# Kernel tuning notes

Hardware: AMD Instinct MI355X
Metric: run time of the kernel (lower is better)

## Reference

```python
import jax, jax.numpy as jnp
import numpy as np
from math import sqrt

D_MODEL = 1024
HEADS = 16
D_K = D_MODEL // HEADS
NEG = -1e9


def setup_inputs() -> dict:
    key = jax.random.key(0)
    ks = jax.random.split(key, 8)
    bs, s, d = 2, 2048, D_MODEL
    inp = {
        "k": jax.random.normal(ks[0], (bs, s, d), jnp.float32),
        "v": jax.random.normal(ks[1], (bs, s, d), jnp.float32),
        "q": jax.random.normal(ks[2], (bs, s, d), jnp.float32),
        "mask": jax.random.randint(ks[3], (bs, s, 1), 0, 2).astype(jnp.int64),
        # torch nn.Linear weights: y = x @ W.T, W is [out, in]
        "Wq": jax.random.normal(ks[4], (d, d), jnp.float32) / sqrt(d),
        "Wk": jax.random.normal(ks[5], (d, d), jnp.float32) / sqrt(d),
        "Wv": jax.random.normal(ks[6], (d, d), jnp.float32) / sqrt(d),
        "Wo": jax.random.normal(ks[7], (d, d), jnp.float32) / sqrt(d),
    }
    return inp


def reference(k, v, q, mask, Wq, Wk, Wv, Wo):
    bs, s_k, d = k.shape
    s_q = q.shape[1]
    h, d_k = HEADS, D_K
    # linear projections (no bias), then split heads -> [bs, h, s, d_k]
    kh = (k @ Wk.T).reshape(bs, s_k, h, d_k).transpose(0, 2, 1, 3)
    vh = (v @ Wv.T).reshape(bs, s_k, h, d_k).transpose(0, 2, 1, 3)
    qh = (q @ Wq.T).reshape(bs, s_q, h, d_k).transpose(0, 2, 1, 3)
    # scaled dot-product scores [bs, h, s_q, s_k]
    scores = jnp.einsum("bhqd,bhkd->bhqk", qh, kh) / sqrt(d_k)
    # mask [bs, s_k, 1] -> [bs, 1, 1, s_k], masked positions get -1e9
    m = mask[:, None].transpose(0, 1, 3, 2)  # [bs,1,1,s_k]
    scores = jnp.where(m == 0, NEG, scores)
    probs = jax.nn.softmax(scores, axis=-1)  # dropout is identity (eval)
    attn = jnp.einsum("bhqk,bhkd->bhqd", probs, vh)
    attn_concat = attn.transpose(0, 2, 1, 3).reshape(bs, s_q, d)
    return attn_concat @ Wo.T
```

## Files before the change

kernel.cpp:

```cpp
#include <hip/hip_runtime.h>

typedef __bf16 bf16x8 __attribute__((ext_vector_type(8)));
typedef float f32x4 __attribute__((ext_vector_type(4)));

#define BS 2
#define SEQ 2048
#define DM 1024
#define NH 16
#define DKH 64
#define GM 4096
#define GN 1024
#define GK 1024
#define NEGV (-1e9f)

#define OFF_XQ 0u
#define OFF_XK 4194304u
#define OFF_XV 8388608u
#define OFF_WQ 12582912u
#define OFF_WK 13631488u
#define OFF_WV 14680064u
#define OFF_WO 15728640u
#define OFF_QH 16777216u
#define OFF_KC 20971520u
#define OFF_VT 25165824u
#define OFF_AT OFF_XQ

#if __has_builtin(__builtin_amdgcn_exp2f)
#define EXP2(x) __builtin_amdgcn_exp2f(x)
#else
static __device__ __forceinline__ float EXP2(float x) {
    float r;
    asm volatile("v_exp_f32 %0, %1" : "=v"(r) : "v"(x));
    return r;
}
#endif

__device__ __forceinline__ unsigned cvt_pk(float lo, float hi) {
    unsigned r;
    asm volatile("v_cvt_pk_bf16_f32 %0, %1, %2" : "=v"(r) : "v"(lo), "v"(hi));
    return r;
}

__device__ __forceinline__ unsigned short f2b(float f) {
    unsigned u = __builtin_bit_cast(unsigned, f);
    u += 0x7fffu + ((u >> 16) & 1u);
    return (unsigned short)(u >> 16);
}

typedef const __attribute__((address_space(1))) unsigned int* gas_t;
typedef __attribute__((address_space(3))) unsigned int* las_t;

__device__ __forceinline__ void gload_lds16(const ushort* g, ushort* l) {
    __builtin_amdgcn_global_load_lds((gas_t)(const void*)g, (las_t)(void*)l, 16, 0, 0);
}

#define BARRIER() __builtin_amdgcn_s_barrier()
#define VMCNT(n) asm volatile("s_waitcnt vmcnt(" #n ")" ::: "memory")

__global__ __launch_bounds__(256)
void cvt_kernel(const float* __restrict__ q, const float* __restrict__ k,
                const float* __restrict__ v, const float* __restrict__ wq,
                const float* __restrict__ wk, const float* __restrict__ wv,
                const float* __restrict__ wo, ushort* __restrict__ ws)
{
    const float* src; unsigned n; unsigned dst;
    switch (blockIdx.y) {
        case 0: src = q;  n = 4194304u; dst = OFF_XQ; break;
        case 1: src = k;  n = 4194304u; dst = OFF_XK; break;
        case 2: src = v;  n = 4194304u; dst = OFF_XV; break;
        case 3: src = wq; n = 1048576u; dst = OFF_WQ; break;
        case 4: src = wk; n = 1048576u; dst = OFF_WK; break;
        case 5: src = wv; n = 1048576u; dst = OFF_WV; break;
        default: src = wo; n = 1048576u; dst = OFF_WO; break;
    }
    unsigned i = (blockIdx.x * 256u + threadIdx.x) * 4u;
    if (i >= n) return;
    float4 f = *(const float4*)(src + i);
    ushort4 o;
    o.x = f2b(f.x); o.y = f2b(f.y); o.z = f2b(f.z); o.w = f2b(f.w);
    *(ushort4*)(ws + dst + i) = o;
}

__global__ __launch_bounds__(256)
void scan_kernel(const int* __restrict__ mask, int* __restrict__ cpos, int* __restrict__ mbuf)
{
    const int b = blockIdx.x;
    const int* mp = mask + (size_t)b * SEQ;
    const int tid = threadIdx.x;
    const int lane = tid & 63, w = tid >> 6;
    int v[8];
    int cnt = 0;
#pragma unroll
    for (int j = 0; j < 8; ++j) { v[j] = mp[tid * 8 + j]; cnt += (v[j] != 0); }
    int inc = cnt;
#pragma unroll
    for (int d = 1; d < 64; d <<= 1) {
        int t = __shfl_up(inc, d);
        if (lane >= d) inc += t;
    }
    __shared__ int wsum[4];
    if (lane == 63) wsum[w] = inc;
    __syncthreads();
    int base = inc - cnt;
    for (int i = 0; i < w; ++i) base += wsum[i];
    int c = base;
    int* ob = cpos + (size_t)b * SEQ;
#pragma unroll
    for (int j = 0; j < 8; ++j) {
        ob[tid * 8 + j] = (v[j] != 0) ? c : -1;
        c += (v[j] != 0);
    }
    if (tid == 255) mbuf[b] = base + cnt;
}

__global__ __launch_bounds__(512)
void gemm256(const ushort* __restrict__ Abase, const ushort* __restrict__ Bbase,
             ushort* __restrict__ wsbase, const int* __restrict__ cpos)
{
    __shared__ __align__(16) ushort lA[2][2][8192];
    __shared__ __align__(16) ushort lB[2][2][8192];

    const unsigned z = blockIdx.z;
    const ushort* A  = Abase + (size_t)z * (GM * GK);
    const ushort* Bw = Bbase + (size_t)z * (GN * GK);
    const float scale = (z == 0) ? 0.125f * 1.44269504088896f : 1.0f;

    const int tid = threadIdx.x;
    const int lane = tid & 63, wid = tid >> 6;
    const int wr = wid >> 2, wc = wid & 3;
    const int lr = lane & 15, lg = lane >> 4;
    const int srow8 = lane >> 3, scol = lane & 7;

    const int lin = blockIdx.y * 4 + blockIdx.x;
    const int xcd = lin & 7, kidx = lin >> 3;
    const int m0 = (xcd * 2 + (kidx >> 2)) * 256;
    const int n0 = (kidx & 3) * 256;

    f32x4 acc[8][4] = {};
    bf16x8 aq[4][2], aq2[4][2], b01[2][2], b23[2][2];

#define STAGE_A(s, h, t)                                                          \
    _Pragma("unroll") for (int c = 0; c < 2; ++c) {                               \
        int rih = (wid * 2 + c) * 8 + srow8;                                      \
        gload_lds16(A + (size_t)(m0 + (h) * 128 + rih) * GK + (t) * 64 +          \
                        ((scol ^ (rih & 7)) * 8),                                 \
                    &lA[s][h][(wid * 2 + c) * 512]);                              \
    }
#define STAGE_B(s, h, t)                                                          \
    _Pragma("unroll") for (int c = 0; c < 2; ++c) {                               \
        int rih = (wid * 2 + c) * 8 + srow8;                                      \
        gload_lds16(Bw + (size_t)(n0 + (h) * 128 + rih) * GK + (t) * 64 +         \
                         ((scol ^ (rih & 7)) * 8),                                \
                    &lB[s][h][(wid * 2 + c) * 512]);                              \
    }
#define LDA_FRAG(dst, s, ibase)                                                   \
    _Pragma("unroll") for (int i2 = 0; i2 < 4; ++i2)                              \
    _Pragma("unroll") for (int kk = 0; kk < 2; ++kk) {                            \
        int row = ((ibase) + i2) * 16 + lr;                                       \
        dst[i2][kk] = *(const bf16x8*)&lA[s][wr][row * 64 +                       \
                          (((kk * 4 + lg) ^ (row & 7)) * 8)];                     \
    }
#define LDB_FRAG(dst, s, jbase)                                                   \
    _Pragma("unroll") for (int j2 = 0; j2 < 2; ++j2)                              \
    _Pragma("unroll") for (int kk = 0; kk < 2; ++kk) {                            \
        int row = (wc & 1) * 64 + ((jbase) + j2) * 16 + lr;                       \
        dst[j2][kk] = *(const bf16x8*)&lB[s][wc >> 1][row * 64 +                  \
                          (((kk * 4 + lg) ^ (row & 7)) * 8)];                     \
    }
#define MMA_Q(ibase, jbase, av, bv)                                               \
    __builtin_amdgcn_s_setprio(1);                                                \
    _Pragma("unroll") for (int i2 = 0; i2 < 4; ++i2)                              \
    _Pragma("unroll") for (int j2 = 0; j2 < 2; ++j2)                              \
    _Pragma("unroll") for (int kk = 0; kk < 2; ++kk)                              \
        acc[(ibase) + i2][(jbase) + j2] = __builtin_amdgcn_mfma_f32_16x16x32_bf16(\
            av[i2][kk], bv[j2][kk], acc[(ibase) + i2][(jbase) + j2], 0, 0, 0);    \
    __builtin_amdgcn_s_setprio(0);

    STAGE_B(0, 0, 0); STAGE_B(0, 1, 0); STAGE_A(0, 0, 0); STAGE_A(0, 1, 0);
    STAGE_B(1, 0, 1); STAGE_B(1, 1, 1); STAGE_A(1, 0, 1); STAGE_A(1, 1, 1);
    VMCNT(8);
    BARRIER();

    for (int it = 0; it < 7; ++it) {
        const int t2 = 2 * it + 2, t3 = 2 * it + 3;
        LDA_FRAG(aq, 0, 0); LDB_FRAG(b01, 0, 0);
        BARRIER(); MMA_Q(0, 0, aq, b01); BARRIER();
        LDB_FRAG(b23, 0, 2);
        BARRIER(); MMA_Q(0, 2, aq, b23); BARRIER();
        LDA_FRAG(aq2, 0, 4);
        STAGE_B(0, 0, t2); STAGE_B(0, 1, t2);
        BARRIER(); MMA_Q(4, 2, aq2, b23); BARRIER();
        STAGE_A(0, 0, t2);
        VMCNT(6);
        BARRIER(); MMA_Q(4, 0, aq2, b01); BARRIER();
        LDA_FRAG(aq, 1, 0); LDB_FRAG(b01, 1, 0);
        STAGE_A(0, 1, t2);
        BARRIER(); MMA_Q(0, 0, aq, b01); BARRIER();
        LDB_FRAG(b23, 1, 2);
        BARRIER(); MMA_Q(0, 2, aq, b23); BARRIER();
        LDA_FRAG(aq2, 1, 4);
        STAGE_B(1, 0, t3); STAGE_B(1, 1, t3);
        BARRIER(); MMA_Q(4, 2, aq2, b23); BARRIER();
        STAGE_A(1, 0, t3); STAGE_A(1, 1, t3);
        VMCNT(8);
        BARRIER(); MMA_Q(4, 0, aq2, b01); BARRIER();
    }

    LDA_FRAG(aq, 0, 0); LDB_FRAG(b01, 0, 0);
    BARRIER(); MMA_Q(0, 0, aq, b01); BARRIER();
    LDB_FRAG(b23, 0, 2);
    BARRIER(); MMA_Q(0, 2, aq, b23); BARRIER();
    LDA_FRAG(aq2, 0, 4);
    BARRIER(); MMA_Q(4, 2, aq2, b23); BARRIER();
    VMCNT(0);
    BARRIER(); MMA_Q(4, 0, aq2, b01); BARRIER();
    LDA_FRAG(aq, 1, 0); LDB_FRAG(b01, 1, 0);
    BARRIER(); MMA_Q(0, 0, aq, b01); BARRIER();
    LDB_FRAG(b23, 1, 2);
    BARRIER(); MMA_Q(0, 2, aq, b23); BARRIER();
    LDA_FRAG(aq2, 1, 4);
    BARRIER(); MMA_Q(4, 2, aq2, b23); BARRIER();
    BARRIER(); MMA_Q(4, 0, aq2, b01); BARRIER();

    ushort* qh  = wsbase + OFF_QH;
    ushort* kc  = wsbase + OFF_KC;
    ushort* vtp = wsbase + OFF_VT;
#pragma unroll
    for (int i = 0; i < 8; ++i) {
#pragma unroll
        for (int r = 0; r < 4; ++r) {
            int row = m0 + wr * 128 + i * 16 + lg * 4 + r;
            int b = row >> 11, s = row & 2047;
            if (z == 0) {
#pragma unroll
                for (int j = 0; j < 4; ++j) {
                    int col = n0 + wc * 64 + j * 16 + lr;
                    qh[(((size_t)b * NH + (col >> 6)) * SEQ + s) * DKH + (col & 63)] =
                        f2b(acc[i][j][r] * scale);
                }
            } else {
                int c = cpos[b * SEQ + s];
                if (c >= 0) {
                    if (z == 1) {
#pragma unroll
                        for (int j = 0; j < 4; ++j) {
                            int col = n0 + wc * 64 + j * 16 + lr;
                            kc[(((size_t)b * NH + (col >> 6)) * SEQ + c) * DKH + (col & 63)] =
                                f2b(acc[i][j][r]);
                        }
                    } else {
                        int vt = (c & ~63) | ((c & 15) * 4 + ((c >> 4) & 3));
#pragma unroll
                        for (int j = 0; j < 4; ++j) {
                            int col = n0 + wc * 64 + j * 16 + lr;
                            vtp[(((size_t)b * NH + (col >> 6)) * DKH + (col & 63)) * SEQ + vt] =
                                f2b(acc[i][j][r]);
                        }
                    }
                }
            }
        }
    }
#undef STAGE_A
#undef STAGE_B
#undef LDA_FRAG
#undef LDB_FRAG
#undef MMA_Q
}

__global__ __launch_bounds__(256)
void gemm_bt(const ushort* __restrict__ A, const ushort* __restrict__ Bw,
             float* __restrict__ of)
{
    __shared__ __align__(16) ushort lA[128 * 64];
    __shared__ __align__(16) ushort lB[128 * 64];

    const int tid = threadIdx.x;
    const int lane = tid & 63, wid = tid >> 6;
    const int wr = wid >> 1, wc = wid & 1;
    const int lr = lane & 15, lg = lane >> 4;
    const int lin = blockIdx.y * 8 + blockIdx.x;
    const int swz = (lin & 7) * 32 + (lin >> 3);
    const int m0 = (swz >> 3) * 128, n0 = (swz & 7) * 128;
    const int srow = wid * 32 + (lane >> 3);
    const int scol = (lane & 7) * 8;

    f32x4 acc[4][4] = {};

    for (int k0 = 0; k0 < GK; k0 += 64) {
        __syncthreads();
#pragma unroll
        for (int p = 0; p < 4; ++p) {
            gload_lds16(A + (size_t)(m0 + srow + p * 8) * GK + k0 + scol,
                        &lA[(wid * 32 + p * 8) * 64]);
            gload_lds16(Bw + (size_t)(n0 + srow + p * 8) * GK + k0 + scol,
                        &lB[(wid * 32 + p * 8) * 64]);
        }
        __syncthreads();
#pragma unroll
        for (int kk = 0; kk < 2; ++kk) {
            bf16x8 af[4], bfr[4];
#pragma unroll
            for (int i = 0; i < 4; ++i) {
                af[i]  = *(const bf16x8*)(&lA[(wr * 64 + i * 16 + lr) * 64 + kk * 32 + lg * 8]);
                bfr[i] = *(const bf16x8*)(&lB[(wc * 64 + i * 16 + lr) * 64 + kk * 32 + lg * 8]);
            }
#pragma unroll
            for (int i = 0; i < 4; ++i)
#pragma unroll
                for (int j = 0; j < 4; ++j)
                    acc[i][j] = __builtin_amdgcn_mfma_f32_16x16x32_bf16(af[i], bfr[j], acc[i][j], 0, 0, 0);
        }
    }

#pragma unroll
    for (int i = 0; i < 4; ++i)
#pragma unroll
        for (int j = 0; j < 4; ++j) {
            int col = n0 + wc * 64 + j * 16 + lr;
#pragma unroll
            for (int r = 0; r < 4; ++r) {
                int row = m0 + wr * 64 + i * 16 + lg * 4 + r;
                of[(size_t)row * GN + col] = acc[i][j][r];
            }
        }
}

__global__ __launch_bounds__(256)
void attn_kernel(ushort* __restrict__ ws, const int* __restrict__ mbuf)
{
    const int bid = blockIdx.x;
    const int qt = bid & 15;
    const int h  = (bid >> 4) & 15;
    const int b  = bid >> 8;
    const int bh = b * NH + h;

    const ushort* Qp = ws + OFF_QH + (size_t)bh * (SEQ * DKH);
    const ushort* Kc = ws + OFF_KC + (size_t)bh * (SEQ * DKH);
    const ushort* VT = ws + OFF_VT + (size_t)bh * (DKH * SEQ);
    ushort* At = ws + OFF_AT;

    const int mb = mbuf[b];
    const int nt = (mb + 63) >> 6;

    __shared__ __align__(16) ushort lK[2][64 * 64];
    __shared__ __align__(16) ushort lV[2][64 * 64];
    __shared__ __align__(16) ushort lP[4][32][72];

    const int tid = threadIdx.x;
    const int lane = tid & 63, wid = tid >> 6;
    const int lr = lane & 15, lg = lane >> 4;
    ushort* lPw = &lP[wid][0][0];

    const int srow = wid * 16 + (lane >> 3);
    const int sg = lane & 7;

    const int qrow0 = qt * 128 + wid * 32;
    bf16x8 qf[2][2];
#pragma unroll
    for (int fr = 0; fr < 2; ++fr)
#pragma unroll
        for (int kk = 0; kk < 2; ++kk)
            qf[fr][kk] = *(const bf16x8*)(Qp + (size_t)(qrow0 + fr * 16 + lr) * DKH + kk * 32 + lg * 8);

    f32x4 acc_o[2][4] = {};
    float lrun[2][4] = {};

    auto STAGE = [&](int buf, int kt) {
        const int kbase = kt * 64;
#pragma unroll
        for (int c = 0; c < 2; ++c) {
            int r = srow + c * 8;
            gload_lds16(Kc + (size_t)(kbase + r) * DKH + ((sg ^ (r & 7)) * 8),
                        &lK[buf][(wid * 16 + c * 8) * 64]);
            gload_lds16(VT + (size_t)r * SEQ + kbase + ((sg ^ (r & 7)) * 8),
                        &lV[buf][(wid * 16 + c * 8) * 64]);
        }
    };

    STAGE(0, 0);
    __syncthreads();

    for (int kt = 0; kt < nt; ++kt) {
        const int cur = kt & 1;
        if (kt + 1 < nt) STAGE(cur ^ 1, kt + 1);
        const ushort* lKc = lK[cur];
        const ushort* lVc = lV[cur];

        f32x4 s[2][4];
        __builtin_amdgcn_s_setprio(1);
#pragma unroll
        for (int fc = 0; fc < 4; ++fc) {
            int row = fc * 16 + lr;
            int sw = row & 7;
            bf16x8 kf0 = *(const bf16x8*)(lKc + row * 64 + ((lg ^ sw) * 8));
            bf16x8 kf1 = *(const bf16x8*)(lKc + row * 64 + (((4 + lg) ^ sw) * 8));
#pragma unroll
            for (int fr = 0; fr < 2; ++fr) {
                f32x4 t = {};
                t = __builtin_amdgcn_mfma_f32_16x16x32_bf16(qf[fr][0], kf0, t, 0, 0, 0);
                t = __builtin_amdgcn_mfma_f32_16x16x32_bf16(qf[fr][1], kf1, t, 0, 0, 0);
                s[fr][fc] = t;
            }
        }
        __builtin_amdgcn_s_setprio(0);

        if (kt == nt - 1) {
            const int kbase = kt * 64;
#pragma unroll
            for (int fc = 0; fc < 4; ++fc)
                if (kbase + fc * 16 + lr >= mb)
#pragma unroll
                    for (int fr = 0; fr < 2; ++fr)
                        s[fr][fc] = f32x4{NEGV, NEGV, NEGV, NEGV};
        }

#pragma unroll
        for (int fr = 0; fr < 2; ++fr)
#pragma unroll
            for (int r = 0; r < 4; ++r) {
                float p0 = EXP2(s[fr][0][r]), p1 = EXP2(s[fr][1][r]);
                float p2 = EXP2(s[fr][2][r]), p3 = EXP2(s[fr][3][r]);
                lrun[fr][r] += (p0 + p1) + (p2 + p3);
                uint2 pk;
                pk.x = cvt_pk(p0, p1);
                pk.y = cvt_pk(p2, p3);
                *(uint2*)(lPw + (fr * 16 + lg * 4 + r) * 72 + lr * 4) = pk;
            }

        __builtin_amdgcn_s_setprio(1);
#pragma unroll
        for (int kk = 0; kk < 2; ++kk) {
            bf16x8 pf[2];
#pragma unroll
            for (int fr = 0; fr < 2; ++fr)
                pf[fr] = *(const bf16x8*)(lPw + (fr * 16 + lr) * 72 + kk * 32 + lg * 8);
#pragma unroll
            for (int fc2 = 0; fc2 < 4; ++fc2) {
                int d = fc2 * 16 + lr;
                bf16x8 vf = *(const bf16x8*)(lVc + d * 64 + (((kk * 4 + lg) ^ (d & 7)) * 8));
#pragma unroll
                for (int fr = 0; fr < 2; ++fr)
                    acc_o[fr][fc2] = __builtin_amdgcn_mfma_f32_16x16x32_bf16(pf[fr], vf, acc_o[fr][fc2], 0, 0, 0);
            }
        }
        __builtin_amdgcn_s_setprio(0);
        __syncthreads();
    }

#pragma unroll
    for (int fr = 0; fr < 2; ++fr)
#pragma unroll
        for (int r = 0; r < 4; ++r) {
            float l = lrun[fr][r];
            l += __shfl_xor(l, 1);
            l += __shfl_xor(l, 2);
            l += __shfl_xor(l, 4);
            l += __shfl_xor(l, 8);
            float rl = 1.0f / l;
            int qrow = qrow0 + fr * 16 + lg * 4 + r;
#pragma unroll
            for (int fc2 = 0; fc2 < 4; ++fc2)
                At[((size_t)(b * SEQ) + qrow) * DM + h * DKH + fc2 * 16 + lr] =
                    f2b(acc_o[fr][fc2][r] * rl);
        }
}

extern "C" void kernel_launch(void* const* d_in, const int* in_sizes, int n_in,
                              void* d_out, int out_size, void* d_ws, size_t ws_size,
                              hipStream_t stream) {
    const float* kin = (const float*)d_in[0];
    const float* vin = (const float*)d_in[1];
    const float* qin = (const float*)d_in[2];
    const int*   msk = (const int*)d_in[3];
    const float* wq  = (const float*)d_in[4];
    const float* wk  = (const float*)d_in[5];
    const float* wv  = (const float*)d_in[6];
    const float* wo  = (const float*)d_in[7];
    ushort* ws = (ushort*)d_ws;
    float* out = (float*)d_out;
    int* cposb = (int*)d_out;
    int* mbuf = cposb + BS * SEQ;

    scan_kernel<<<2, 256, 0, stream>>>(msk, cposb, mbuf);
    cvt_kernel<<<dim3(4096, 7), 256, 0, stream>>>(qin, kin, vin, wq, wk, wv, wo, ws);
    gemm256<<<dim3(4, 16, 3), 512, 0, stream>>>(ws + OFF_XQ, ws + OFF_WQ, ws, cposb);
    attn_kernel<<<512, 256, 0, stream>>>(ws, mbuf);
    gemm_bt<<<dim3(8, 32), 256, 0, stream>>>(ws + OFF_AT, ws + OFF_WO, out);
}
```

Measured before the change: 128.6 us.

## Fuse mask scan into convert kernel and load attention K/V directly from global

Merges the mask prefix-scan into the fp32-to-bf16 conversion kernel as an extra grid row, which removes one launch, and widens conversion to 8 elements per thread using packed conversion. The attention kernel drops LDS staging of K and V, the double buffering and the per-tile barriers, and instead reads MFMA fragments straight from global memory, relying on cache reuse. It also swizzles the block index so that co-scheduled blocks share heads, and removes the setprio hints. Reading K/V directly from global trades LDS traffic and synchronisation for possibly higher-latency global loads that are not software pipelined.

After: 168.1 us. 1.31x slower.

```diff
diff --git a/kernel.cpp b/kernel.cpp
--- a/kernel.cpp
+++ b/kernel.cpp
@@ -58,11 +58,44 @@
 #define VMCNT(n) asm volatile("s_waitcnt vmcnt(" #n ")" ::: "memory")
 
 __global__ __launch_bounds__(256)
-void cvt_kernel(const float* __restrict__ q, const float* __restrict__ k,
-                const float* __restrict__ v, const float* __restrict__ wq,
-                const float* __restrict__ wk, const float* __restrict__ wv,
-                const float* __restrict__ wo, ushort* __restrict__ ws)
+void cvt_scan(const float* __restrict__ q, const float* __restrict__ k,
+              const float* __restrict__ v, const float* __restrict__ wq,
+              const float* __restrict__ wk, const float* __restrict__ wv,
+              const float* __restrict__ wo, ushort* __restrict__ ws,
+              const int* __restrict__ mask, int* __restrict__ cpos,
+              int* __restrict__ mbuf)
 {
+    const int tid = threadIdx.x;
+    if (blockIdx.y == 7) {
+        if (blockIdx.x >= 2) return;
+        const int b = blockIdx.x;
+        const int* mp = mask + (size_t)b * SEQ;
+        const int lane = tid & 63, w = tid >> 6;
+        int vv[8];
+        int cnt = 0;
+#pragma unroll
+        for (int j = 0; j < 8; ++j) { vv[j] = mp[tid * 8 + j]; cnt += (vv[j] != 0); }
+        int inc = cnt;
+#pragma unroll
+        for (int d = 1; d < 64; d <<= 1) {
+            int t = __shfl_up(inc, d);
+            if (lane >= d) inc += t;
+        }
+        __shared__ int wsum[4];
+        if (lane == 63) wsum[w] = inc;
+        __syncthreads();
+        int base = inc - cnt;
+        for (int i = 0; i < w; ++i) base += wsum[i];
+        int c = base;
+        int* ob = cpos + (size_t)b * SEQ;
+#pragma unroll
+        for (int j = 0; j < 8; ++j) {
+            ob[tid * 8 + j] = (vv[j] != 0) ? c : -1;
+            c += (vv[j] != 0);
+        }
+        if (tid == 255) mbuf[b] = base + cnt;
+        return;
+    }
     const float* src; unsigned n; unsigned dst;
     switch (blockIdx.y) {
         case 0: src = q;  n = 4194304u; dst = OFF_XQ; break;
@@ -73,44 +106,16 @@
         case 5: src = wv; n = 1048576u; dst = OFF_WV; break;
         default: src = wo; n = 1048576u; dst = OFF_WO; break;
     }
-    unsigned i = (blockIdx.x * 256u + threadIdx.x) * 4u;
+    unsigned i = (blockIdx.x * 256u + tid) * 8u;
     if (i >= n) return;
-    float4 f = *(const float4*)(src + i);
-    ushort4 o;
-    o.x = f2b(f.x); o.y = f2b(f.y); o.z = f2b(f.z); o.w = f2b(f.w);
-    *(ushort4*)(ws + dst + i) = o;
-}
-
-__global__ __launch_bounds__(256)
-void scan_kernel(const int* __restrict__ mask, int* __restrict__ cpos, int* __restrict__ mbuf)
-{
-    const int b = blockIdx.x;
-    const int* mp = mask + (size_t)b * SEQ;
-    const int tid = threadIdx.x;
-    const int lane = tid & 63, w = tid >> 6;
-    int v[8];
-    int cnt = 0;
-#pragma unroll
-    for (int j = 0; j < 8; ++j) { v[j] = mp[tid * 8 + j]; cnt += (v[j] != 0); }
-    int inc = cnt;
-#pragma unroll
-    for (int d = 1; d < 64; d <<= 1) {
-        int t = __shfl_up(inc, d);
-        if (lane >= d) inc += t;
-    }
-    __shared__ int wsum[4];
-    if (lane == 63) wsum[w] = inc;
-    __syncthreads();
-    int base = inc - cnt;
-    for (int i = 0; i < w; ++i) base += wsum[i];
-    int c = base;
-    int* ob = cpos + (size_t)b * SEQ;
-#pragma unroll
-    for (int j = 0; j < 8; ++j) {
-        ob[tid * 8 + j] = (v[j] != 0) ? c : -1;
-        c += (v[j] != 0);
-    }
-    if (tid == 255) mbuf[b] = base + cnt;
+    float4 f0 = *(const float4*)(src + i);
+    float4 f1 = *(const float4*)(src + i + 4);
+    uint4 o;
+    o.x = cvt_pk(f0.x, f0.y);
+    o.y = cvt_pk(f0.z, f0.w);
+    o.z = cvt_pk(f1.x, f1.y);
+    o.w = cvt_pk(f1.z, f1.w);
+    *(uint4*)(ws + dst + i) = o;
 }
 
 __global__ __launch_bounds__(512)
@@ -330,9 +335,10 @@
 void attn_kernel(ushort* __restrict__ ws, const int* __restrict__ mbuf)
 {
     const int bid = blockIdx.x;
-    const int qt = bid & 15;
-    const int h  = (bid >> 4) & 15;
-    const int b  = bid >> 8;
+    const int swzb = (bid & 7) * 64 + (bid >> 3);
+    const int qt = swzb & 15;
+    const int h  = (swzb >> 4) & 15;
+    const int b  = swzb >> 8;
     const int bh = b * NH + h;
 
     const ushort* Qp = ws + OFF_QH + (size_t)bh * (SEQ * DKH);
@@ -343,8 +349,6 @@
     const int mb = mbuf[b];
     const int nt = (mb + 63) >> 6;
 
-    __shared__ __align__(16) ushort lK[2][64 * 64];
-    __shared__ __align__(16) ushort lV[2][64 * 64];
     __shared__ __align__(16) ushort lP[4][32][72];
 
     const int tid = threadIdx.x;
@@ -352,9 +356,6 @@
     const int lr = lane & 15, lg = lane >> 4;
     ushort* lPw = &lP[wid][0][0];
 
-    const int srow = wid * 16 + (lane >> 3);
-    const int sg = lane & 7;
-
     const int qrow0 = qt * 128 + wid * 32;
     bf16x8 qf[2][2];
 #pragma unroll
@@ -366,35 +367,15 @@
     f32x4 acc_o[2][4] = {};
     float lrun[2][4] = {};
 
-    auto STAGE = [&](int buf, int kt) {
+    for (int kt = 0; kt < nt; ++kt) {
         const int kbase = kt * 64;
-#pragma unroll
-        for (int c = 0; c < 2; ++c) {
-            int r = srow + c * 8;
-            gload_lds16(Kc + (size_t)(kbase + r) * DKH + ((sg ^ (r & 7)) * 8),
-                        &lK[buf][(wid * 16 + c * 8) * 64]);
-            gload_lds16(VT + (size_t)r * SEQ + kbase + ((sg ^ (r & 7)) * 8),
-                        &lV[buf][(wid * 16 + c * 8) * 64]);
-        }
-    };
-
-    STAGE(0, 0);
-    __syncthreads();
-
-    for (int kt = 0; kt < nt; ++kt) {
-        const int cur = kt & 1;
-        if (kt + 1 < nt) STAGE(cur ^ 1, kt + 1);
-        const ushort* lKc = lK[cur];
-        const ushort* lVc = lV[cur];
 
         f32x4 s[2][4];
-        __builtin_amdgcn_s_setprio(1);
 #pragma unroll
         for (int fc = 0; fc < 4; ++fc) {
-            int row = fc * 16 + lr;
-            int sw = row & 7;
-            bf16x8 kf0 = *(const bf16x8*)(lKc + row * 64 + ((lg ^ sw) * 8));
-            bf16x8 kf1 = *(const bf16x8*)(lKc + row * 64 + (((4 + lg) ^ sw) * 8));
+            const ushort* krow = Kc + (size_t)(kbase + fc * 16 + lr) * DKH;
+            bf16x8 kf0 = *(const bf16x8*)(krow + lg * 8);
+            bf16x8 kf1 = *(const bf16x8*)(krow + 32 + lg * 8);
 #pragma unroll
             for (int fr = 0; fr < 2; ++fr) {
                 f32x4 t = {};
@@ -403,10 +384,8 @@
                 s[fr][fc] = t;
             }
         }
-        __builtin_amdgcn_s_setprio(0);
 
         if (kt == nt - 1) {
-            const int kbase = kt * 64;
 #pragma unroll
             for (int fc = 0; fc < 4; ++fc)
                 if (kbase + fc * 16 + lr >= mb)
@@ -428,7 +407,6 @@
                 *(uint2*)(lPw + (fr * 16 + lg * 4 + r) * 72 + lr * 4) = pk;
             }
 
-        __builtin_amdgcn_s_setprio(1);
 #pragma unroll
         for (int kk = 0; kk < 2; ++kk) {
             bf16x8 pf[2];
@@ -437,15 +415,12 @@
                 pf[fr] = *(const bf16x8*)(lPw + (fr * 16 + lr) * 72 + kk * 32 + lg * 8);
 #pragma unroll
             for (int fc2 = 0; fc2 < 4; ++fc2) {
-                int d = fc2 * 16 + lr;
-                bf16x8 vf = *(const bf16x8*)(lVc + d * 64 + (((kk * 4 + lg) ^ (d & 7)) * 8));
+                bf16x8 vf = *(const bf16x8*)(VT + (size_t)(fc2 * 16 + lr) * SEQ + kbase + (kk * 4 + lg) * 8);
 #pragma unroll
                 for (int fr = 0; fr < 2; ++fr)
                     acc_o[fr][fc2] = __builtin_amdgcn_mfma_f32_16x16x32_bf16(pf[fr], vf, acc_o[fr][fc2], 0, 0, 0);
             }
         }
-        __builtin_amdgcn_s_setprio(0);
-        __syncthreads();
     }
 
 #pragma unroll
@@ -482,8 +457,8 @@
     int* cposb = (int*)d_out;
     int* mbuf = cposb + BS * SEQ;
 
-    scan_kernel<<<2, 256, 0, stream>>>(msk, cposb, mbuf);
-    cvt_kernel<<<dim3(4096, 7), 256, 0, stream>>>(qin, kin, vin, wq, wk, wv, wo, ws);
+    cvt_scan<<<dim3(2048, 8), 256, 0, stream>>>(qin, kin, vin, wq, wk, wv, wo,
+                                                ws, msk, cposb, mbuf);
     gemm256<<<dim3(4, 16, 3), 512, 0, stream>>>(ws + OFF_XQ, ws + OFF_WQ, ws, cposb);
     attn_kernel<<<512, 256, 0, stream>>>(ws, mbuf);
     gemm_bt<<<dim3(8, 32), 256, 0, stream>>>(ws + OFF_AT, ws + OFF_WO, out);
```
